# Kernel tuning notes

Hardware: AMD Instinct MI355X
Metric: run time of the kernel (lower is better)

## Reference

```python
import jax, jax.numpy as jnp
import numpy as np

D = 128        # dim
S = 64         # seq_len
NSYM = 128     # symbols
STACK = 16     # stack_size
DEPTH = 8      # max_depth (ACT recursion)
THRESH = 0.99  # act_threshold
EPS = 1e-6
RES = 0.1      # residual_weight
LAM_E = 0.01   # lambda_energy
TEMP = 1.0
B = 512


def _clin(xr, xi, Wr, Wi):
    # ComplexLinear: (Wr + i Wi)(xr + i xi)
    return xr @ Wr.T - xi @ Wi.T, xr @ Wi.T + xi @ Wr.T


def _cattn(zr, zi, wr, wi):
    # ComplexAttention: complex QKV projections, real softmax over concat(real,imag)
    qr, qi = _clin(zr, zi, wr[0], wi[0])
    kr, ki = _clin(zr, zi, wr[1], wi[1])
    vr, vi = _clin(zr, zi, wr[2], wi[2])
    qf = jnp.concatenate([qr, qi], -1)
    kf = jnp.concatenate([kr, ki], -1)
    a = jax.nn.softmax(jnp.einsum('bsd,btd->bst', qf, kf) * (D ** -0.5), axis=-1)
    return jnp.einsum('bst,btd->bsd', a, vr), jnp.einsum('bst,btd->bsd', a, vi)


def setup_inputs() -> dict:
    key = jax.random.key(0)
    ks = jax.random.split(key, 12)
    sc = 1.0 / np.sqrt(D)
    return {
        'z_real': jax.random.normal(ks[0], (B, S, D), jnp.float32),
        'z_imag': jax.random.normal(ks[1], (B, S, D), jnp.float32),
        'attn_wr': jax.random.normal(ks[2], (3, D, D), jnp.float32) * sc,
        'attn_wi': jax.random.normal(ks[3], (3, D, D), jnp.float32) * sc,
        'mem_wr': jax.random.normal(ks[4], (3, D, D), jnp.float32) * sc,
        'mem_wi': jax.random.normal(ks[5], (3, D, D), jnp.float32) * sc,
        'ctrl_w': jax.random.normal(ks[6], (2 * D, 3), jnp.float32) * sc,
        'ctrl_b': jnp.zeros((3,), jnp.float32),
        'halt_w': jax.random.normal(ks[7], (2 * D, 1), jnp.float32) * sc,
        'halt_b': jnp.zeros((1,), jnp.float32),
        'codebook': jax.random.normal(ks[8], (NSYM, 2 * D), jnp.float32) * 0.2,
        'adjacency': jax.random.normal(ks[9], (NSYM, NSYM), jnp.float32),
    }


def reference(z_real, z_imag, attn_wr, attn_wi, mem_wr, mem_wi,
              ctrl_w, ctrl_b, halt_w, halt_b, codebook, adjacency):
    b = z_real.shape[0]
    mem0 = jnp.zeros((b, STACK, 2 * D), z_real.dtype)
    ptr0 = jnp.zeros((b, STACK), z_real.dtype).at[:, 0].set(1.0)
    probs0 = jnp.zeros((b, NSYM), z_real.dtype)
    halt0 = jnp.zeros((b,), z_real.dtype)
    acc0 = jnp.zeros((b, S, 2 * D), z_real.dtype)

    def step(carry, t):
        zr, zi, mem, ptr, prev_probs, halt_acc, acc = carry
        # --- complex self-attention with residual recursion ---
        ar, ai = _cattn(zr, zi, attn_wr, attn_wi)
        zr = ar + RES * zr
        zi = ai + RES * zi
        # --- memory stack (push/pop/stay pointer machine) ---
        zf = jnp.concatenate([zr.mean(1), zi.mean(1)], -1)  # [B, 2D]
        g = jax.nn.sigmoid(zf @ ctrl_w + ctrl_b)
        tot = g.sum(-1, keepdims=True) + EPS
        push, pop, stay = g[:, 0:1] / tot, g[:, 1:2] / tot, g[:, 2:3] / tot
        ptr = push * jnp.roll(ptr, 1, axis=1) + pop * jnp.roll(ptr, -1, axis=1) + stay * ptr
        mem = mem * (1 - push[..., None]) + push[..., None] * zf[:, None, :]
        amr, ami = _cattn(mem[..., :D], mem[..., D:], mem_wr, mem_wi)
        read = (jnp.concatenate([amr, ami], -1) * ptr[..., None]).sum(1)  # [B, 2D]
        zr = zr + RES * read[:, None, :D]
        zi = zi + RES * read[:, None, D:]
        # --- grounded graph VQ: codebook distance + adjacency energy bias ---
        zf = jnp.concatenate([zr.mean(1), zi.mean(1)], -1)
        d = ((zf ** 2).sum(-1, keepdims=True) + (codebook ** 2).sum(-1)
             - 2 * zf @ codebook.T) / (2 * D)
        mag = jnp.sqrt(zr ** 2 + zi ** 2)
        up = jax.nn.softplus(mag.var() / (1.0 + EPS))  # complexity modulation
        gb = prev_probs @ adjacency
        d_tot = jnp.where(t == 0, d, d - LAM_E * up * jax.nn.sigmoid(gb))
        probs = jax.nn.softmax(-d_tot / TEMP, axis=-1)
        quant = probs @ codebook
        zr = zr + RES * quant[:, None, :D]
        zi = zi + RES * quant[:, None, D:]
        # --- ACT halting accumulation ---
        p = jax.nn.sigmoid(zf @ halt_w + halt_b)[:, 0]
        running = (halt_acc < THRESH).astype(zr.dtype)
        w = jnp.where(halt_acc + p * running >= THRESH, 1.0 - halt_acc, p) * running
        halt_acc = halt_acc + w
        acc = acc + w[:, None, None] * jnp.concatenate([zr, zi], -1)
        return (zr, zi, mem, ptr, probs, halt_acc, acc), None

    carry, _ = jax.lax.scan(step, (z_real, z_imag, mem0, ptr0, probs0, halt0, acc0),
                            jnp.arange(DEPTH))
    return carry[6]  # ACT-weighted state, [B, S, 2D]
```

## Files before the change

### kernel.cpp

```cpp
#include <hip/hip_runtime.h>
#include <math.h>

#define BB 512
#define SS 64
#define DD 128
#define FF 256
#define NSYM 128
#define STK 16
#define NDEPTH 8

typedef _Float16 half_t;
typedef __attribute__((ext_vector_type(4))) _Float16 half4;
typedef __attribute__((ext_vector_type(8))) _Float16 half8;
typedef __attribute__((ext_vector_type(4))) float f32x4;

#define Z_OFF      0ull
#define QKV_OFF    8388608ull
#define ZFW_OFF    33554432ull
#define MV_OFF     35651584ull
#define SIG_OFF    35782656ull
#define ZF1_OFF    41951232ull
#define ZF2_OFF    42082304ull
#define READ_OFF   42213376ull
#define PROBS_OFF  42344448ull
#define DELTA_OFF  42409984ull
#define HALT_OFF   42541056ull
#define PVAL_OFF   42541568ull
#define WACT_OFF   42542080ull
#define MAGP_OFF   42542592ull
#define MQKV_OFF   42740224ull
#define CB2_OFF    42936832ull

__global__ void k_buildwt32(const float* __restrict__ wr, const float* __restrict__ wi,
                            float* __restrict__ WT32) {
    int idx = blockIdx.x * 256 + threadIdx.x;
    if (idx >= 768 * 256) return;
    int col = idx >> 8;
    int e   = idx & 255;
    int h   = col >> 8;
    int c   = col & 255;
    const float* Wr = wr + h * DD * DD;
    const float* Wi = wi + h * DD * DD;
    float v;
    if (c < DD) {
        v = (e < DD) ? Wr[c * DD + e] : -Wi[c * DD + (e - DD)];
    } else {
        int j = c - DD;
        v = (e < DD) ? Wi[j * DD + e] : Wr[j * DD + (e - DD)];
    }
    WT32[idx] = v;
}

__global__ __launch_bounds__(256) void k_buildG(const float* __restrict__ WT32,
                                                half_t* __restrict__ GTh,
                                                half_t* __restrict__ GTl) {
    __shared__ float kcol[256];
    int n = blockIdx.x;
    int e = threadIdx.x;
    kcol[e] = WT32[65536 + e * 256 + n];
    __syncthreads();
    float s = 0.f;
    for (int c = 0; c < 256; ++c) s += kcol[c] * WT32[c * 256 + e];
    half_t h = (half_t)s;
    GTh[n * 256 + e] = h;
    GTl[n * 256 + e] = (half_t)(s - (float)h);
}

__global__ void k_splitWv(const float* __restrict__ WT32,
                          half_t* __restrict__ WvTh, half_t* __restrict__ WvTl) {
    int idx = blockIdx.x * 256 + threadIdx.x;
    float v = WT32[131072 + idx];
    half_t h = (half_t)v;
    WvTh[idx] = h;
    WvTl[idx] = (half_t)(v - (float)h);
}

__global__ void k_cb2(const float* __restrict__ cb, float* __restrict__ cb2) {
    int n = threadIdx.x;
    float s = 0.f;
    for (int c = 0; c < FF; ++c) { float v = cb[n * FF + c]; s += v * v; }
    cb2[n] = s;
}

__global__ __launch_bounds__(256) void k_init(const float* __restrict__ zr_in,
                                              const float* __restrict__ zi_in,
                                              float* __restrict__ z, float* __restrict__ mv,
                                              float* __restrict__ sigma,
                                              float* __restrict__ halt, float* __restrict__ acc,
                                              float* __restrict__ delta, float* __restrict__ wact) {
    size_t idx = (size_t)blockIdx.x * 256 + threadIdx.x;
    int c = (int)(idx & 255);
    size_t bs = idx >> 8;
    z[idx] = (c < DD) ? zr_in[bs * DD + c] : zi_in[bs * DD + (c - DD)];
    acc[idx] = 0.f;
    if (idx < 131072) { mv[idx] = 0.f; delta[idx] = 0.f; }
    if (idx < 512)   { halt[idx] = 0.f; wact[idx] = 0.f; sigma[idx] = 1.f; }
}

__global__ __launch_bounds__(512, 1) void k_attn8(
        float* __restrict__ z,
        const half_t* __restrict__ GTh, const half_t* __restrict__ GTl,
        const half_t* __restrict__ WvTh, const half_t* __restrict__ WvTl,
        const float* __restrict__ delta, const float* __restrict__ wact,
        float* __restrict__ acc, float* __restrict__ zf1g) {
    __shared__ half_t Zh[16896];
    __shared__ half_t Zl[16896];
    __shared__ half_t Ubuf[2][18432];
    __shared__ half_t Pbuf[2][4][1152];

    int b = blockIdx.x, tid = threadIdx.x;
    int w = tid >> 6, lane = tid & 63;
    int l15 = lane & 15, lq = lane >> 4;
    float* zb = z + (size_t)b * (SS * FF);
    float* accb = acc + (size_t)b * (SS * FF);

    float wa = wact[b];
    f32x4 dv = *(const f32x4*)(delta + b * FF + lane * 4);
    bool doacc = (wa != 0.0f);
#pragma unroll
    for (int it = 0; it < 8; ++it) {
        int i = w * 8 + it;
        f32x4 zv = *(const f32x4*)(zb + (size_t)i * FF + lane * 4);
        f32x4 x0;
#pragma unroll
        for (int jj = 0; jj < 4; ++jj) x0[jj] = zv[jj] + 0.1f * dv[jj];
        if (doacc) {
            f32x4 av = *(const f32x4*)(accb + (size_t)i * FF + lane * 4);
#pragma unroll
            for (int jj = 0; jj < 4; ++jj) av[jj] += wa * x0[jj];
            *(f32x4*)(accb + (size_t)i * FF + lane * 4) = av;
        }
        half4 h4, l4;
#pragma unroll
        for (int jj = 0; jj < 4; ++jj) {
            half_t h = (half_t)x0[jj];
            h4[jj] = h; l4[jj] = (half_t)(x0[jj] - (float)h);
        }
        *(half4*)&Zh[i * 264 + lane * 4] = h4;
        *(half4*)&Zl[i * 264 + lane * 4] = l4;
    }
    __syncthreads();

    {
        f32x4 tac[4][2];
#pragma unroll
        for (int mt = 0; mt < 4; ++mt)
#pragma unroll
            for (int nt = 0; nt < 2; ++nt) tac[mt][nt] = (f32x4){0.f, 0.f, 0.f, 0.f};
        __builtin_amdgcn_s_setprio(1);
#pragma unroll 2
        for (int kt = 0; kt < 8; ++kt) {
            int kc = kt * 32 + lq * 8;
            half8 ah[4], al[4], gh[2], gl[2];
#pragma unroll
            for (int mt = 0; mt < 4; ++mt) {
                int ro = (mt * 16 + l15) * 264 + kc;
                ah[mt] = *(const half8*)&Zh[ro];
                al[mt] = *(const half8*)&Zl[ro];
            }
#pragma unroll
            for (int nt = 0; nt < 2; ++nt) {
                size_t go = (size_t)(w * 32 + nt * 16 + l15) * 256 + kc;
                gh[nt] = *(const half8*)(GTh + go);
                gl[nt] = *(const half8*)(GTl + go);
            }
#pragma unroll
            for (int mt = 0; mt < 4; ++mt)
#pragma unroll
                for (int nt = 0; nt < 2; ++nt) {
                    tac[mt][nt] = __builtin_amdgcn_mfma_f32_16x16x32_f16(ah[mt], gh[nt], tac[mt][nt], 0, 0, 0);
                    tac[mt][nt] = __builtin_amdgcn_mfma_f32_16x16x32_f16(ah[mt], gl[nt], tac[mt][nt], 0, 0, 0);
                    tac[mt][nt] = __builtin_amdgcn_mfma_f32_16x16x32_f16(al[mt], gh[nt], tac[mt][nt], 0, 0, 0);
                }
        }
        __builtin_amdgcn_s_setprio(0);
        const float scale = 0.08838834764831845f;
#pragma unroll
        for (int mt = 0; mt < 4; ++mt)
#pragma unroll
            for (int nt = 0; nt < 2; ++nt)
#pragma unroll
                for (int r = 0; r < 4; ++r) {
                    int m = mt * 16 + lq * 4 + r;
                    int n = w * 32 + nt * 16 + l15;
                    float v = tac[mt][nt][r] * scale;
                    half_t h = (half_t)v;
                    Ubuf[0][m * 264 + n] = h;
                    Ubuf[1][m * 264 + n] = (half_t)(v - (float)h);
                }
    }
    __syncthreads();

    if (w < 4) {
        f32x4 sac[4];
#pragma unroll
        for (int jt = 0; jt < 4; ++jt) sac[jt] = (f32x4){0.f, 0.f, 0.f, 0.f};
        __builtin_amdgcn_s_setprio(1);
#pragma unroll 2
        for (int kt = 0; kt < 8; ++kt) {
            int kc = kt * 32 + lq * 8;
            int to = (w * 16 + l15) * 264 + kc;
            half8 bh = *(const half8*)&Ubuf[0][to];
            half8 bl = *(const half8*)&Ubuf[1][to];
            half8 ah[4], al[4];
#pragma unroll
            for (int jt = 0; jt < 4; ++jt) {
                int ro = (jt * 16 + l15) * 264 + kc;
                ah[jt] = *(const half8*)&Zh[ro];
                al[jt] = *(const half8*)&Zl[ro];
            }
#pragma unroll
            for (int jt = 0; jt < 4; ++jt) {
                sac[jt] = __builtin_amdgcn_mfma_f32_16x16x32_f16(ah[jt], bh, sac[jt], 0, 0, 0);
                sac[jt] = __builtin_amdgcn_mfma_f32_16x16x32_f16(ah[jt], bl, sac[jt], 0, 0, 0);
                sac[jt] = __builtin_amdgcn_mfma_f32_16x16x32_f16(al[jt], bh, sac[jt], 0, 0, 0);
            }
        }
        __builtin_amdgcn_s_setprio(0);
        float sv[4][4];
        float mx = -1e30f;
#pragma unroll
        for (int jt = 0; jt < 4; ++jt)
#pragma unroll
            for (int r = 0; r < 4; ++r) { sv[jt][r] = sac[jt][r]; mx = fmaxf(mx, sv[jt][r]); }
        mx = fmaxf(mx, __shfl_xor(mx, 16));
        mx = fmaxf(mx, __shfl_xor(mx, 32));
        float ssum = 0.f;
#pragma unroll
        for (int jt = 0; jt < 4; ++jt)
#pragma unroll
            for (int r = 0; r < 4; ++r) { float e = expf(sv[jt][r] - mx); sv[jt][r] = e; ssum += e; }
        ssum += __shfl_xor(ssum, 16);
        ssum += __shfl_xor(ssum, 32);
        float inv = 1.f / ssum;
#pragma unroll
        for (int jt = 0; jt < 4; ++jt) {
            half4 h4, l4;
#pragma unroll
            for (int r = 0; r < 4; ++r) {
                float pv = sv[jt][r] * inv;
                half_t hh = (half_t)pv;
                h4[r] = hh;
                l4[r] = (half_t)(pv - (float)hh);
            }
            *(half4*)&Pbuf[0][w][l15 * 72 + jt * 16 + lq * 4] = h4;
            *(half4*)&Pbuf[1][w][l15 * 72 + jt * 16 + lq * 4] = l4;
        }
    }

    f32x4 vac[4][2];
#pragma unroll
    for (int mt = 0; mt < 4; ++mt)
#pragma unroll
        for (int nt = 0; nt < 2; ++nt) vac[mt][nt] = (f32x4){0.f, 0.f, 0.f, 0.f};
    __builtin_amdgcn_s_setprio(1);
#pragma unroll 2
    for (int kt = 0; kt < 8; ++kt) {
        int kc = kt * 32 + lq * 8;
        half8 ah[4], al[4], gh[2], gl[2];
#pragma unroll
        for (int mt = 0; mt < 4; ++mt) {
            int ro = (mt * 16 + l15) * 264 + kc;
            ah[mt] = *(const half8*)&Zh[ro];
            al[mt] = *(const half8*)&Zl[ro];
        }
#pragma unroll
        for (int nt = 0; nt < 2; ++nt) {
            size_t go = (size_t)(w * 32 + nt * 16 + l15) * 256 + kc;
            gh[nt] = *(const half8*)(WvTh + go);
            gl[nt] = *(const half8*)(WvTl + go);
        }
#pragma unroll
        for (int mt = 0; mt < 4; ++mt)
#pragma unroll
            for (int nt = 0; nt < 2; ++nt) {
                vac[mt][nt] = __builtin_amdgcn_mfma_f32_16x16x32_f16(ah[mt], gh[nt], vac[mt][nt], 0, 0, 0);
                vac[mt][nt] = __builtin_amdgcn_mfma_f32_16x16x32_f16(ah[mt], gl[nt], vac[mt][nt], 0, 0, 0);
                vac[mt][nt] = __builtin_amdgcn_mfma_f32_16x16x32_f16(al[mt], gh[nt], vac[mt][nt], 0, 0, 0);
            }
    }
    __builtin_amdgcn_s_setprio(0);
    __syncthreads();

#pragma unroll
    for (int mt = 0; mt < 4; ++mt)
#pragma unroll
        for (int nt = 0; nt < 2; ++nt) {
            int n = w * 32 + nt * 16 + l15;
            int m0 = mt * 16 + lq * 4;
            half4 h4, l4;
#pragma unroll
            for (int r = 0; r < 4; ++r) {
                float v = vac[mt][nt][r];
                half_t h = (half_t)v;
                h4[r] = h; l4[r] = (half_t)(v - (float)h);
            }
            *(half4*)&Ubuf[0][n * 72 + m0] = h4;
            *(half4*)&Ubuf[1][n * 72 + m0] = l4;
        }
    __syncthreads();

    f32x4 oc[4][2];
#pragma unroll
    for (int mt = 0; mt < 4; ++mt)
#pragma unroll
        for (int nt = 0; nt < 2; ++nt) oc[mt][nt] = (f32x4){0.f, 0.f, 0.f, 0.f};
    __builtin_amdgcn_s_setprio(1);
#pragma unroll
    for (int kt = 0; kt < 2; ++kt) {
        half8 pah[4], pal[4];
#pragma unroll
        for (int mt = 0; mt < 4; ++mt) {
            int po = l15 * 72 + kt * 32 + lq * 8;
            pah[mt] = *(const half8*)&Pbuf[0][mt][po];
            pal[mt] = *(const half8*)&Pbuf[1][mt][po];
        }
#pragma unroll
        for (int nt = 0; nt < 2; ++nt) {
            int n = w * 32 + nt * 16 + l15;
            half8 vbh = *(const half8*)&Ubuf[0][n * 72 + kt * 32 + lq * 8];
            half8 vbl = *(const half8*)&Ubuf[1][n * 72 + kt * 32 + lq * 8];
#pragma unroll
            for (int mt = 0; mt < 4; ++mt) {
                oc[mt][nt] = __builtin_amdgcn_mfma_f32_16x16x32_f16(pah[mt], vbh, oc[mt][nt], 0, 0, 0);
                oc[mt][nt] = __builtin_amdgcn_mfma_f32_16x16x32_f16(pah[mt], vbl, oc[mt][nt], 0, 0, 0);
                oc[mt][nt] = __builtin_amdgcn_mfma_f32_16x16x32_f16(pal[mt], vbh, oc[mt][nt], 0, 0, 0);
            }
        }
    }
    __builtin_amdgcn_s_setprio(0);

    float zfs[2] = {0.f, 0.f};
#pragma unroll
    for (int mt = 0; mt < 4; ++mt)
#pragma unroll
        for (int nt = 0; nt < 2; ++nt)
#pragma unroll
            for (int r = 0; r < 4; ++r) {
                int i = mt * 16 + lq * 4 + r;
                int c = w * 32 + nt * 16 + l15;
                int zo = i * 264 + c;
                float x0 = (float)Zh[zo] + (float)Zl[zo];
                float z1 = oc[mt][nt][r] + 0.1f * x0;
                zb[(size_t)i * FF + c] = z1;
                zfs[nt] += z1;
            }
#pragma unroll
    for (int nt = 0; nt < 2; ++nt) {
        zfs[nt] += __shfl_xor(zfs[nt], 16);
        zfs[nt] += __shfl_xor(zfs[nt], 32);
    }
    if (lq == 0) {
#pragma unroll
        for (int nt = 0; nt < 2; ++nt)
            zf1g[b * FF + w * 32 + nt * 16 + l15] = zfs[nt] * (1.f / 64.f);
    }
}

__global__ __launch_bounds__(256) void gemm_v(const float* __restrict__ A,
                                              const half_t* __restrict__ WTh,
                                              const half_t* __restrict__ WTl,
                                              float* __restrict__ C) {
    __shared__ float As[128][36];
    int bm = blockIdx.x >> 1;
    int bn = blockIdx.x & 1;
    int tid = threadIdx.x;
    int w = tid >> 6;
    int lane = tid & 63;
    int wr = w >> 1, wc = w & 1;
    int l15 = lane & 15;
    int lq  = lane >> 4;

    f32x4 acc[4][4];
#pragma unroll
    for (int i = 0; i < 4; ++i)
#pragma unroll
        for (int j = 0; j < 4; ++j) acc[i][j] = (f32x4){0.f, 0.f, 0.f, 0.f};

    const float* Ablk = A + (size_t)bm * 128 * 256;
    int colbase = bn * 128 + wc * 64;

    int srow = tid >> 1;
    int sseg = (tid & 1) * 16;

    for (int k0 = 0; k0 < 256; k0 += 32) {
        __syncthreads();
        {
            const float* src = Ablk + (size_t)srow * 256 + k0 + sseg;
            f32x4 v0 = *(const f32x4*)(src);
            f32x4 v1 = *(const f32x4*)(src + 4);
            f32x4 v2 = *(const f32x4*)(src + 8);
            f32x4 v3 = *(const f32x4*)(src + 12);
            *(f32x4*)&As[srow][sseg]      = v0;
            *(f32x4*)&As[srow][sseg + 4]  = v1;
            *(f32x4*)&As[srow][sseg + 8]  = v2;
            *(f32x4*)&As[srow][sseg + 12] = v3;
        }
        __syncthreads();

        half8 bh[4], bl[4];
#pragma unroll
        for (int tj = 0; tj < 4; ++tj) {
            size_t off = (size_t)(colbase + tj * 16 + l15) * 256 + k0 + lq * 8;
            bh[tj] = *(const half8*)(WTh + off);
            bl[tj] = *(const half8*)(WTl + off);
        }

        half8 ah[4], al[4];
#pragma unroll
        for (int ti = 0; ti < 4; ++ti) {
            const float* ap = &As[wr * 64 + ti * 16 + l15][lq * 8];
            f32x4 a0 = *(const f32x4*)(ap);
            f32x4 a1 = *(const f32x4*)(ap + 4);
#pragma unroll
            for (int j = 0; j < 4; ++j) {
                float x = a0[j];
                half_t h = (half_t)x;
                ah[ti][j] = h;
                al[ti][j] = (half_t)(x - (float)h);
            }
#pragma unroll
            for (int j = 0; j < 4; ++j) {
                float x = a1[j];
                half_t h = (half_t)x;
                ah[ti][4 + j] = h;
                al[ti][4 + j] = (half_t)(x - (float)h);
            }
        }

#pragma unroll
        for (int ti = 0; ti < 4; ++ti)
#pragma unroll
            for (int tj = 0; tj < 4; ++tj)
                acc[ti][tj] = __builtin_amdgcn_mfma_f32_16x16x32_f16(ah[ti], bh[tj], acc[ti][tj], 0, 0, 0);
#pragma unroll
        for (int ti = 0; ti < 4; ++ti)
#pragma unroll
            for (int tj = 0; tj < 4; ++tj)
                acc[ti][tj] = __builtin_amdgcn_mfma_f32_16x16x32_f16(ah[ti], bl[tj], acc[ti][tj], 0, 0, 0);
#pragma unroll
        for (int ti = 0; ti < 4; ++ti)
#pragma unroll
            for (int tj = 0; tj < 4; ++tj)
                acc[ti][tj] = __builtin_amdgcn_mfma_f32_16x16x32_f16(al[ti], bh[tj], acc[ti][tj], 0, 0, 0);
    }

    float* Cb = C + (size_t)(bm * 128 + wr * 64) * 256 + bn * 128 + wc * 64;
#pragma unroll
    for (int ti = 0; ti < 4; ++ti)
#pragma unroll
        for (int tj = 0; tj < 4; ++tj) {
            int r0 = ti * 16 + lq * 4;
            int c0 = tj * 16 + l15;
#pragma unroll
            for (int r = 0; r < 4; ++r)
                Cb[(size_t)(r0 + r) * 256 + c0] = acc[ti][tj][r];
        }
}

__global__ __launch_bounds__(256) void k_stack3(
        const float* __restrict__ zf1,
        const float* __restrict__ ctrl_w, const float* __restrict__ ctrl_b,
        float* __restrict__ sigma, float* __restrict__ mv,
        const float* __restrict__ zfWv,
        float* __restrict__ readv, float* __restrict__ zf2,
        const float* __restrict__ halt_w, const float* __restrict__ halt_b,
        float* __restrict__ pval,
        const float* __restrict__ z, float* __restrict__ magpart) {
    __shared__ float zf[256];
    __shared__ float g[3];
    __shared__ float rd[256];
    __shared__ float red[256];

    int b = blockIdx.x, tid = threadIdx.x;
    int w = tid >> 6, lane = tid & 63;

    zf[tid] = zf1[b * FF + tid];
    __syncthreads();
    if (w < 3) {
        float s = 0.f;
#pragma unroll
        for (int q = 0; q < 4; ++q) {
            int c = lane + 64 * q;
            s += zf[c] * ctrl_w[c * 3 + w];
        }
#pragma unroll
        for (int off = 1; off < 64; off <<= 1) s += __shfl_xor(s, off);
        if (lane == 0) g[w] = 1.f / (1.f + expf(-(s + ctrl_b[w])));
    }
    __syncthreads();
    float tot = g[0] + g[1] + g[2] + 1e-6f;
    float push = g[0] / tot, pop = g[1] / tot, stay = g[2] / tot;
    float signew = sigma[b] * (push + pop + stay);
    if (tid == 0) sigma[b] = signew;

    float omp = 1.f - push;
    float m2v = mv[b * FF + tid] * omp + push * zfWv[b * FF + tid];
    mv[b * FF + tid] = m2v;

    float a = signew * m2v;
    rd[tid] = a;
    readv[b * FF + tid] = a;
    float z2 = zf[tid] + 0.1f * a;
    zf2[b * FF + tid] = z2;
    red[tid] = z2 * halt_w[tid];
    __syncthreads();
    for (int off = 128; off > 0; off >>= 1) {
        if (tid < off) red[tid] += red[tid + off];
        __syncthreads();
    }
    if (tid == 0) pval[b] = 1.f / (1.f + expf(-(red[0] + halt_b[0])));
    __syncthreads();

    {
        int d = tid & 127, hf = tid >> 7;
        float rr = 0.1f * rd[d];
        float ri = 0.1f * rd[DD + d];
        const float* zb = z + (size_t)b * (SS * FF);
        float ms = 0.f, msq = 0.f;
        for (int s32 = 0; s32 < 32; ++s32) {
            int s = hf * 32 + s32;
            float zr = zb[s * FF + d] + rr;
            float zi = zb[s * FF + DD + d] + ri;
            float m2 = zr * zr + zi * zi;
            ms += sqrtf(m2); msq += m2;
        }
        red[tid] = ms;
        __syncthreads();
        for (int off = 128; off > 0; off >>= 1) {
            if (tid < off) red[tid] += red[tid + off];
            __syncthreads();
        }
        float tms = red[0];
        __syncthreads();
        red[tid] = msq;
        __syncthreads();
        for (int off = 128; off > 0; off >>= 1) {
            if (tid < off) red[tid] += red[tid + off];
            __syncthreads();
        }
        if (tid == 0) { magpart[2 * b] = tms; magpart[2 * b + 1] = red[0]; }
    }
}

__global__ __launch_bounds__(256) void k_vq2(
        const float* __restrict__ zf2g, const float* __restrict__ readv,
        float* __restrict__ probs, float* __restrict__ halt,
        const float* __restrict__ pvalg, const float* __restrict__ magp,
        const float* __restrict__ cb, const float* __restrict__ cb2,
        const float* __restrict__ adj,
        float* __restrict__ delta, float* __restrict__ wact, int t) {
    __shared__ float zf[256];
    __shared__ float pr[128];
    __shared__ float upred[8];
    __shared__ float zzred[4];
    __shared__ float mxred[4];
    __shared__ float sered[4];

    int b = blockIdx.x, tid = threadIdx.x;
    int w = tid >> 6, lane = tid & 63;

    zf[tid] = zf2g[b * FF + tid];

    float up = 0.f;
    if (t > 0) {
        f32x4 mv4 = *(const f32x4*)(magp + tid * 4);
        float pa = mv4[0] + mv4[2];
        float pb = mv4[1] + mv4[3];
#pragma unroll
        for (int off = 1; off < 64; off <<= 1) {
            pa += __shfl_xor(pa, off);
            pb += __shfl_xor(pb, off);
        }
        if (lane == 0) { upred[w * 2] = pa; upred[w * 2 + 1] = pb; }
    }
    __syncthreads();
    if (t > 0) {
        float tms  = upred[0] + upred[2] + upred[4] + upred[6];
        float tmsq = upred[1] + upred[3] + upred[5] + upred[7];
        const float N = 4194304.f;
        float mean = tms / N;
        float var = tmsq / N - mean * mean;
        float x = var / (1.f + 1e-6f);
        up = (x > 20.f) ? x : log1pf(expf(x));
    }

    {
        float part = zf[tid] * zf[tid];
#pragma unroll
        for (int off = 1; off < 64; off <<= 1) part += __shfl_xor(part, off);
        if (lane == 0) zzred[w] = part;
    }
    __syncthreads();
    float zz = zzred[0] + zzred[1] + zzred[2] + zzred[3];

    int n = tid >> 1, half = tid & 1;
    float dacc = 0.f;
    {
        const float* cbn = cb + n * FF + half * 128;
        const float* zfp = zf + half * 128;
#pragma unroll 8
        for (int c2 = 0; c2 < 128; c2 += 4) {
            f32x4 cv = *(const f32x4*)(cbn + c2);
            dacc += cv[0] * zfp[c2] + cv[1] * zfp[c2 + 1] + cv[2] * zfp[c2 + 2] + cv[3] * zfp[c2 + 3];
        }
        dacc += __shfl_xor(dacc, 1);
    }
    float gacc = 0.f;
    if (t > 0) {
        const float* pp = probs + b * NSYM;
        for (int k = half * 64; k < half * 64 + 64; ++k)
            gacc += pp[k] * adj[k * NSYM + n];
        gacc += __shfl_xor(gacc, 1);
    }

    float dist = (zz + cb2[n] - 2.f * dacc) * (1.f / 256.f);
    float dtot = dist;
    if (t > 0) dtot = dist - 0.01f * up * (1.f / (1.f + expf(-gacc)));
    float vval = -dtot;

    {
        float m = vval;
#pragma unroll
        for (int off = 1; off < 64; off <<= 1) m = fmaxf(m, __shfl_xor(m, off));
        if (lane == 0) mxred[w] = m;
    }
    __syncthreads();
    float mx = fmaxf(fmaxf(mxred[0], mxred[1]), fmaxf(mxred[2], mxred[3]));

    float e = expf(vval - mx);
    {
        float s = (half == 0) ? e : 0.f;
#pragma unroll
        for (int off = 1; off < 64; off <<= 1) s += __shfl_xor(s, off);
        if (lane == 0) sered[w] = s;
    }
    __syncthreads();
    float se = sered[0] + sered[1] + sered[2] + sered[3];
    float psm = e / se;
    if (half == 0) {
        pr[n] = psm;
        probs[b * NSYM + n] = psm;
    }
    __syncthreads();

    float q = 0.f;
#pragma unroll 4
    for (int k = 0; k < NSYM; ++k) q += pr[k] * cb[k * FF + tid];
    delta[b * FF + tid] = readv[b * FF + tid] + q;

    if (tid == 0) {
        float h = halt[b], p = pvalg[b];
        float running = (h < 0.99f) ? 1.f : 0.f;
        float w2 = (((h + p * running) >= 0.99f) ? (1.f - h) : p) * running;
        halt[b] = h + w2;
        wact[b] = w2;
    }
}

__global__ __launch_bounds__(256) void k_epilogue(const float* __restrict__ z,
                                                  const float* __restrict__ delta,
                                                  const float* __restrict__ wact,
                                                  float* __restrict__ acc) {
    int idx = blockIdx.x * 256 + threadIdx.x;
    int b = idx >> 14;
    int c = idx & 255;
    float wa = wact[b];
    if (wa != 0.0f)
        acc[idx] += wa * (z[idx] + 0.1f * delta[b * FF + c]);
}

extern "C" void kernel_launch(void* const* d_in, const int* in_sizes, int n_in,
                              void* d_out, int out_size, void* d_ws, size_t ws_size,
                              hipStream_t stream) {
    const float* z_real  = (const float*)d_in[0];
    const float* z_imag  = (const float*)d_in[1];
    const float* attn_wr = (const float*)d_in[2];
    const float* attn_wi = (const float*)d_in[3];
    const float* mem_wr  = (const float*)d_in[4];
    const float* mem_wi  = (const float*)d_in[5];
    const float* ctrl_w  = (const float*)d_in[6];
    const float* ctrl_b  = (const float*)d_in[7];
    const float* halt_w  = (const float*)d_in[8];
    const float* halt_b  = (const float*)d_in[9];
    const float* codebook  = (const float*)d_in[10];
    const float* adjacency = (const float*)d_in[11];

    float* ws = (float*)d_ws;
    float* z      = ws + Z_OFF;
    float* WT32   = ws + QKV_OFF;
    half_t* GTh   = (half_t*)(ws + QKV_OFF + 196608);
    half_t* GTl   = GTh + 65536;
    half_t* WvTh  = GTl + 65536;
    half_t* WvTl  = WvTh + 65536;
    float* zfWv   = ws + ZFW_OFF;
    half_t* MvTh  = (half_t*)(ws + ZFW_OFF + 131072);
    half_t* MvTl  = MvTh + 65536;
    float* mv     = ws + MV_OFF;
    float* sigma  = ws + SIG_OFF;
    float* zf1    = ws + ZF1_OFF;
    float* zf2    = ws + ZF2_OFF;
    float* readv  = ws + READ_OFF;
    float* probs  = ws + PROBS_OFF;
    float* delta  = ws + DELTA_OFF;
    float* halt   = ws + HALT_OFF;
    float* pval   = ws + PVAL_OFF;
    float* wact   = ws + WACT_OFF;
    float* magp   = ws + MAGP_OFF;
    float* MT32   = ws + MQKV_OFF;
    float* cb2    = ws + CB2_OFF;
    float* acc    = (float*)d_out;

    k_buildwt32<<<768, 256, 0, stream>>>(attn_wr, attn_wi, WT32);
    k_buildG<<<256, 256, 0, stream>>>(WT32, GTh, GTl);
    k_splitWv<<<256, 256, 0, stream>>>(WT32, WvTh, WvTl);
    k_buildwt32<<<768, 256, 0, stream>>>(mem_wr, mem_wi, MT32);
    k_splitWv<<<256, 256, 0, stream>>>(MT32, MvTh, MvTl);
    k_cb2<<<1, 128, 0, stream>>>(codebook, cb2);
    k_init<<<32768, 256, 0, stream>>>(z_real, z_imag, z, mv, sigma, halt, acc,
                                      delta, wact);

    for (int t = 0; t < NDEPTH; ++t) {
        k_attn8<<<BB, 512, 0, stream>>>(z, GTh, GTl, WvTh, WvTl, delta, wact, acc, zf1);
        gemm_v<<<8, 256, 0, stream>>>(zf1, MvTh, MvTl, zfWv);
        k_stack3<<<BB, 256, 0, stream>>>(zf1, ctrl_w, ctrl_b, sigma, mv, zfWv,
                                         readv, zf2, halt_w, halt_b, pval, z, magp);
        k_vq2<<<BB, 256, 0, stream>>>(zf2, readv, probs, halt, pval, magp,
                                      codebook, cb2, adjacency, delta, wact, t);
    }
    k_epilogue<<<32768, 256, 0, stream>>>(z, delta, wact, acc);
}
```

Before: 838.0 us.

## Split softmax across all warps, fuse memory-value GEMV into stack kernel, fold epilogue

Attention scores and softmax now use all eight warps. Each handles half the key columns and merges partial max and sum through shared memory, instead of four warps doing the work while the rest idle. The separate fp16-split gemm_v launch for the memory value projection becomes a per-block fp32 GEMV inside k_stack3, using a directly built fp32 weight matrix. The final epilogue accumulation moves into the last k_vq2 launch. These changes aim to cut launches and idle warps, at the cost of a 256x256 FP32 GEMV per batch block in k_stack3 and a serial 64-row loop in the last vq kernel.

```diff
diff --git a/kernel.cpp b/kernel.cpp
--- a/kernel.cpp
+++ b/kernel.cpp
@@ -16,7 +16,7 @@
 
 #define Z_OFF      0ull
 #define QKV_OFF    8388608ull
-#define ZFW_OFF    33554432ull
+#define WVM_OFF    33554432ull
 #define MV_OFF     35651584ull
 #define SIG_OFF    35782656ull
 #define ZF1_OFF    41951232ull
@@ -28,7 +28,6 @@
 #define PVAL_OFF   42541568ull
 #define WACT_OFF   42542080ull
 #define MAGP_OFF   42542592ull
-#define MQKV_OFF   42740224ull
 #define CB2_OFF    42936832ull
 
 __global__ void k_buildwt32(const float* __restrict__ wr, const float* __restrict__ wi,
@@ -75,6 +74,23 @@
     WvTl[idx] = (half_t)(v - (float)h);
 }
 
+__global__ void k_buildWv32m(const float* __restrict__ wr, const float* __restrict__ wi,
+                             float* __restrict__ Wv32m) {
+    int idx = blockIdx.x * 256 + threadIdx.x;
+    int e = idx >> 8;
+    int c = idx & 255;
+    const float* Wr = wr + 2 * DD * DD;
+    const float* Wi = wi + 2 * DD * DD;
+    float v;
+    if (c < DD) {
+        v = (e < DD) ? Wr[c * DD + e] : -Wi[c * DD + (e - DD)];
+    } else {
+        int j = c - DD;
+        v = (e < DD) ? Wi[j * DD + e] : Wr[j * DD + (e - DD)];
+    }
+    Wv32m[idx] = v;
+}
+
 __global__ void k_cb2(const float* __restrict__ cb, float* __restrict__ cb2) {
     int n = threadIdx.x;
     float s = 0.f;
@@ -107,6 +123,8 @@
     __shared__ half_t Zl[16896];
     __shared__ half_t Ubuf[2][18432];
     __shared__ half_t Pbuf[2][4][1152];
+    __shared__ float Smx[4][2][16];
+    __shared__ float Ssum[4][2][16];
 
     int b = blockIdx.x, tid = threadIdx.x;
     int w = tid >> 6, lane = tid & 63;
@@ -191,61 +209,50 @@
     }
     __syncthreads();
 
-    if (w < 4) {
-        f32x4 sac[4];
-#pragma unroll
-        for (int jt = 0; jt < 4; ++jt) sac[jt] = (f32x4){0.f, 0.f, 0.f, 0.f};
+    int qb = w & 3;
+    int jh = w >> 2;
+    float sv[2][4];
+    {
+        f32x4 sac[2];
+        sac[0] = (f32x4){0.f, 0.f, 0.f, 0.f};
+        sac[1] = (f32x4){0.f, 0.f, 0.f, 0.f};
         __builtin_amdgcn_s_setprio(1);
 #pragma unroll 2
         for (int kt = 0; kt < 8; ++kt) {
             int kc = kt * 32 + lq * 8;
-            int to = (w * 16 + l15) * 264 + kc;
+            int to = (qb * 16 + l15) * 264 + kc;
             half8 bh = *(const half8*)&Ubuf[0][to];
             half8 bl = *(const half8*)&Ubuf[1][to];
-            half8 ah[4], al[4];
-#pragma unroll
-            for (int jt = 0; jt < 4; ++jt) {
-                int ro = (jt * 16 + l15) * 264 + kc;
+            half8 ah[2], al[2];
+#pragma unroll
+            for (int jt = 0; jt < 2; ++jt) {
+                int ro = ((jh * 2 + jt) * 16 + l15) * 264 + kc;
                 ah[jt] = *(const half8*)&Zh[ro];
                 al[jt] = *(const half8*)&Zl[ro];
             }
 #pragma unroll
-            for (int jt = 0; jt < 4; ++jt) {
+            for (int jt = 0; jt < 2; ++jt) {
                 sac[jt] = __builtin_amdgcn_mfma_f32_16x16x32_f16(ah[jt], bh, sac[jt], 0, 0, 0);
                 sac[jt] = __builtin_amdgcn_mfma_f32_16x16x32_f16(ah[jt], bl, sac[jt], 0, 0, 0);
                 sac[jt] = __builtin_amdgcn_mfma_f32_16x16x32_f16(al[jt], bh, sac[jt], 0, 0, 0);
             }
         }
         __builtin_amdgcn_s_setprio(0);
-        float sv[4][4];
-        float mx = -1e30f;
-#pragma unroll
-        for (int jt = 0; jt < 4; ++jt)
-#pragma unroll
-            for (int r = 0; r < 4; ++r) { sv[jt][r] = sac[jt][r]; mx = fmaxf(mx, sv[jt][r]); }
-        mx = fmaxf(mx, __shfl_xor(mx, 16));
-        mx = fmaxf(mx, __shfl_xor(mx, 32));
-        float ssum = 0.f;
-#pragma unroll
-        for (int jt = 0; jt < 4; ++jt)
-#pragma unroll
-            for (int r = 0; r < 4; ++r) { float e = expf(sv[jt][r] - mx); sv[jt][r] = e; ssum += e; }
-        ssum += __shfl_xor(ssum, 16);
-        ssum += __shfl_xor(ssum, 32);
-        float inv = 1.f / ssum;
-#pragma unroll
-        for (int jt = 0; jt < 4; ++jt) {
-            half4 h4, l4;
-#pragma unroll
-            for (int r = 0; r < 4; ++r) {
-                float pv = sv[jt][r] * inv;
-                half_t hh = (half_t)pv;
-                h4[r] = hh;
-                l4[r] = (half_t)(pv - (float)hh);
-            }
-            *(half4*)&Pbuf[0][w][l15 * 72 + jt * 16 + lq * 4] = h4;
-            *(half4*)&Pbuf[1][w][l15 * 72 + jt * 16 + lq * 4] = l4;
-        }
+        float mxh = -1e30f;
+#pragma unroll
+        for (int jt = 0; jt < 2; ++jt)
+#pragma unroll
+            for (int r = 0; r < 4; ++r) { sv[jt][r] = sac[jt][r]; mxh = fmaxf(mxh, sv[jt][r]); }
+        mxh = fmaxf(mxh, __shfl_xor(mxh, 16));
+        mxh = fmaxf(mxh, __shfl_xor(mxh, 32));
+        float sumh = 0.f;
+#pragma unroll
+        for (int jt = 0; jt < 2; ++jt)
+#pragma unroll
+            for (int r = 0; r < 4; ++r) { float e = expf(sv[jt][r] - mxh); sv[jt][r] = e; sumh += e; }
+        sumh += __shfl_xor(sumh, 16);
+        sumh += __shfl_xor(sumh, 32);
+        if (lq == 0) { Smx[qb][jh][l15] = mxh; Ssum[qb][jh][l15] = sumh; }
     }
 
     f32x4 vac[4][2];
@@ -281,6 +288,27 @@
     }
     __builtin_amdgcn_s_setprio(0);
     __syncthreads();
+
+    {
+        float mx0 = Smx[qb][0][l15], mx1 = Smx[qb][1][l15];
+        float gmx = fmaxf(mx0, mx1);
+        float ssum = Ssum[qb][0][l15] * expf(mx0 - gmx) + Ssum[qb][1][l15] * expf(mx1 - gmx);
+        float pscale = expf(((jh == 0) ? mx0 : mx1) - gmx) / ssum;
+#pragma unroll
+        for (int jt = 0; jt < 2; ++jt) {
+            half4 h4, l4;
+#pragma unroll
+            for (int r = 0; r < 4; ++r) {
+                float pv = sv[jt][r] * pscale;
+                half_t hh = (half_t)pv;
+                h4[r] = hh;
+                l4[r] = (half_t)(pv - (float)hh);
+            }
+            int po = l15 * 72 + (jh * 2 + jt) * 16 + lq * 4;
+            *(half4*)&Pbuf[0][qb][po] = h4;
+            *(half4*)&Pbuf[1][qb][po] = l4;
+        }
+    }
 
 #pragma unroll
     for (int mt = 0; mt < 4; ++mt)
@@ -357,112 +385,11 @@
     }
 }
 
-__global__ __launch_bounds__(256) void gemm_v(const float* __restrict__ A,
-                                              const half_t* __restrict__ WTh,
-                                              const half_t* __restrict__ WTl,
-                                              float* __restrict__ C) {
-    __shared__ float As[128][36];
-    int bm = blockIdx.x >> 1;
-    int bn = blockIdx.x & 1;
-    int tid = threadIdx.x;
-    int w = tid >> 6;
-    int lane = tid & 63;
-    int wr = w >> 1, wc = w & 1;
-    int l15 = lane & 15;
-    int lq  = lane >> 4;
-
-    f32x4 acc[4][4];
-#pragma unroll
-    for (int i = 0; i < 4; ++i)
-#pragma unroll
-        for (int j = 0; j < 4; ++j) acc[i][j] = (f32x4){0.f, 0.f, 0.f, 0.f};
-
-    const float* Ablk = A + (size_t)bm * 128 * 256;
-    int colbase = bn * 128 + wc * 64;
-
-    int srow = tid >> 1;
-    int sseg = (tid & 1) * 16;
-
-    for (int k0 = 0; k0 < 256; k0 += 32) {
-        __syncthreads();
-        {
-            const float* src = Ablk + (size_t)srow * 256 + k0 + sseg;
-            f32x4 v0 = *(const f32x4*)(src);
-            f32x4 v1 = *(const f32x4*)(src + 4);
-            f32x4 v2 = *(const f32x4*)(src + 8);
-            f32x4 v3 = *(const f32x4*)(src + 12);
-            *(f32x4*)&As[srow][sseg]      = v0;
-            *(f32x4*)&As[srow][sseg + 4]  = v1;
-            *(f32x4*)&As[srow][sseg + 8]  = v2;
-            *(f32x4*)&As[srow][sseg + 12] = v3;
-        }
-        __syncthreads();
-
-        half8 bh[4], bl[4];
-#pragma unroll
-        for (int tj = 0; tj < 4; ++tj) {
-            size_t off = (size_t)(colbase + tj * 16 + l15) * 256 + k0 + lq * 8;
-            bh[tj] = *(const half8*)(WTh + off);
-            bl[tj] = *(const half8*)(WTl + off);
-        }
-
-        half8 ah[4], al[4];
-#pragma unroll
-        for (int ti = 0; ti < 4; ++ti) {
-            const float* ap = &As[wr * 64 + ti * 16 + l15][lq * 8];
-            f32x4 a0 = *(const f32x4*)(ap);
-            f32x4 a1 = *(const f32x4*)(ap + 4);
-#pragma unroll
-            for (int j = 0; j < 4; ++j) {
-                float x = a0[j];
-                half_t h = (half_t)x;
-                ah[ti][j] = h;
-                al[ti][j] = (half_t)(x - (float)h);
-            }
-#pragma unroll
-            for (int j = 0; j < 4; ++j) {
-                float x = a1[j];
-                half_t h = (half_t)x;
-                ah[ti][4 + j] = h;
-                al[ti][4 + j] = (half_t)(x - (float)h);
-            }
-        }
-
-#pragma unroll
-        for (int ti = 0; ti < 4; ++ti)
-#pragma unroll
-            for (int tj = 0; tj < 4; ++tj)
-                acc[ti][tj] = __builtin_amdgcn_mfma_f32_16x16x32_f16(ah[ti], bh[tj], acc[ti][tj], 0, 0, 0);
-#pragma unroll
-        for (int ti = 0; ti < 4; ++ti)
-#pragma unroll
-            for (int tj = 0; tj < 4; ++tj)
-                acc[ti][tj] = __builtin_amdgcn_mfma_f32_16x16x32_f16(ah[ti], bl[tj], acc[ti][tj], 0, 0, 0);
-#pragma unroll
-        for (int ti = 0; ti < 4; ++ti)
-#pragma unroll
-            for (int tj = 0; tj < 4; ++tj)
-                acc[ti][tj] = __builtin_amdgcn_mfma_f32_16x16x32_f16(al[ti], bh[tj], acc[ti][tj], 0, 0, 0);
-    }
-
-    float* Cb = C + (size_t)(bm * 128 + wr * 64) * 256 + bn * 128 + wc * 64;
-#pragma unroll
-    for (int ti = 0; ti < 4; ++ti)
-#pragma unroll
-        for (int tj = 0; tj < 4; ++tj) {
-            int r0 = ti * 16 + lq * 4;
-            int c0 = tj * 16 + l15;
-#pragma unroll
-            for (int r = 0; r < 4; ++r)
-                Cb[(size_t)(r0 + r) * 256 + c0] = acc[ti][tj][r];
-        }
-}
-
 __global__ __launch_bounds__(256) void k_stack3(
         const float* __restrict__ zf1,
         const float* __restrict__ ctrl_w, const float* __restrict__ ctrl_b,
         float* __restrict__ sigma, float* __restrict__ mv,
-        const float* __restrict__ zfWv,
+        const float* __restrict__ Wv32m,
         float* __restrict__ readv, float* __restrict__ zf2,
         const float* __restrict__ halt_w, const float* __restrict__ halt_b,
         float* __restrict__ pval,
@@ -477,6 +404,11 @@
 
     zf[tid] = zf1[b * FF + tid];
     __syncthreads();
+
+    float zw = 0.f;
+#pragma unroll 8
+    for (int e = 0; e < 256; ++e) zw += Wv32m[e * 256 + tid] * zf[e];
+
     if (w < 3) {
         float s = 0.f;
 #pragma unroll
@@ -495,7 +427,7 @@
     if (tid == 0) sigma[b] = signew;
 
     float omp = 1.f - push;
-    float m2v = mv[b * FF + tid] * omp + push * zfWv[b * FF + tid];
+    float m2v = mv[b * FF + tid] * omp + push * zw;
     mv[b * FF + tid] = m2v;
 
     float a = signew * m2v;
@@ -549,13 +481,16 @@
         const float* __restrict__ pvalg, const float* __restrict__ magp,
         const float* __restrict__ cb, const float* __restrict__ cb2,
         const float* __restrict__ adj,
-        float* __restrict__ delta, float* __restrict__ wact, int t) {
+        float* __restrict__ delta, float* __restrict__ wact,
+        const float* __restrict__ z, float* __restrict__ acc,
+        int t, int last) {
     __shared__ float zf[256];
     __shared__ float pr[128];
     __shared__ float upred[8];
     __shared__ float zzred[4];
     __shared__ float mxred[4];
     __shared__ float sered[4];
+    __shared__ float waS[1];
 
     int b = blockIdx.x, tid = threadIdx.x;
     int w = tid >> 6, lane = tid & 63;
@@ -647,7 +582,8 @@
     float q = 0.f;
 #pragma unroll 4
     for (int k = 0; k < NSYM; ++k) q += pr[k] * cb[k * FF + tid];
-    delta[b * FF + tid] = readv[b * FF + tid] + q;
+    float dltc = readv[b * FF + tid] + q;
+    delta[b * FF + tid] = dltc;
 
     if (tid == 0) {
         float h = halt[b], p = pvalg[b];
@@ -655,19 +591,19 @@
         float w2 = (((h + p * running) >= 0.99f) ? (1.f - h) : p) * running;
         halt[b] = h + w2;
         wact[b] = w2;
-    }
-}
-
-__global__ __launch_bounds__(256) void k_epilogue(const float* __restrict__ z,
-                                                  const float* __restrict__ delta,
-                                                  const float* __restrict__ wact,
-                                                  float* __restrict__ acc) {
-    int idx = blockIdx.x * 256 + threadIdx.x;
-    int b = idx >> 14;
-    int c = idx & 255;
-    float wa = wact[b];
-    if (wa != 0.0f)
-        acc[idx] += wa * (z[idx] + 0.1f * delta[b * FF + c]);
+        waS[0] = w2;
+    }
+
+    if (last) {
+        __syncthreads();
+        float wa = waS[0];
+        if (wa != 0.0f) {
+            const float* zb = z + (size_t)b * (SS * FF);
+            float* ab = acc + (size_t)b * (SS * FF);
+            for (int s = 0; s < SS; ++s)
+                ab[s * FF + tid] += wa * (zb[s * FF + tid] + 0.1f * dltc);
+        }
+    }
 }
 
 extern "C" void kernel_launch(void* const* d_in, const int* in_sizes, int n_in,
@@ -693,9 +629,7 @@
     half_t* GTl   = GTh + 65536;
     half_t* WvTh  = GTl + 65536;
     half_t* WvTl  = WvTh + 65536;
-    float* zfWv   = ws + ZFW_OFF;
-    half_t* MvTh  = (half_t*)(ws + ZFW_OFF + 131072);
-    half_t* MvTl  = MvTh + 65536;
+    float* Wv32m  = ws + WVM_OFF;
     float* mv     = ws + MV_OFF;
     float* sigma  = ws + SIG_OFF;
     float* zf1    = ws + ZF1_OFF;
@@ -707,26 +641,23 @@
     float* pval   = ws + PVAL_OFF;
     float* wact   = ws + WACT_OFF;
     float* magp   = ws + MAGP_OFF;
-    float* MT32   = ws + MQKV_OFF;
     float* cb2    = ws + CB2_OFF;
     float* acc    = (float*)d_out;
 
     k_buildwt32<<<768, 256, 0, stream>>>(attn_wr, attn_wi, WT32);
     k_buildG<<<256, 256, 0, stream>>>(WT32, GTh, GTl);
     k_splitWv<<<256, 256, 0, stream>>>(WT32, WvTh, WvTl);
-    k_buildwt32<<<768, 256, 0, stream>>>(mem_wr, mem_wi, MT32);
-    k_splitWv<<<256, 256, 0, stream>>>(MT32, MvTh, MvTl);
+    k_buildWv32m<<<256, 256, 0, stream>>>(mem_wr, mem_wi, Wv32m);
     k_cb2<<<1, 128, 0, stream>>>(codebook, cb2);
     k_init<<<32768, 256, 0, stream>>>(z_real, z_imag, z, mv, sigma, halt, acc,
                                       delta, wact);
 
     for (int t = 0; t < NDEPTH; ++t) {
         k_attn8<<<BB, 512, 0, stream>>>(z, GTh, GTl, WvTh, WvTl, delta, wact, acc, zf1);
-        gemm_v<<<8, 256, 0, stream>>>(zf1, MvTh, MvTl, zfWv);
-        k_stack3<<<BB, 256, 0, stream>>>(zf1, ctrl_w, ctrl_b, sigma, mv, zfWv,
+        k_stack3<<<BB, 256, 0, stream>>>(zf1, ctrl_w, ctrl_b, sigma, mv, Wv32m,
                                          readv, zf2, halt_w, halt_b, pval, z, magp);
         k_vq2<<<BB, 256, 0, stream>>>(zf2, readv, probs, halt, pval, magp,
-                                      codebook, cb2, adjacency, delta, wact, t);
-    }
-    k_epilogue<<<32768, 256, 0, stream>>>(z, delta, wact, acc);
-}
+                                      codebook, cb2, adjacency, delta, wact,
+                                      z, acc, t, (t == NDEPTH - 1) ? 1 : 0);
+    }
+}
```

Result: faster. 781.7 us (-6.7%).
